# Kernel tuning notes

Hardware: AMD Instinct MI355X
Metric: run time of the kernel (lower is better)

Reference implementation:

```python
import jax, jax.numpy as jnp
import numpy as np

B, H, W, C = 16, 256, 256, 32
FILTER = 64


def conv_relu(x, k, b):
    y = jax.lax.conv_general_dilated(x, k, (1, 1), 'VALID',
                                     dimension_numbers=('NHWC', 'HWIO', 'NHWC'))
    return jax.nn.relu(y + b)


def maxpool2(x):
    return jax.lax.reduce_window(x, -jnp.inf, jax.lax.max,
                                 (1, 2, 2, 1), (1, 2, 2, 1), 'VALID')


def affine_grid_generator(theta):
    # tf.meshgrid default 'xy': shapes [W, H]
    xs = jnp.linspace(-1.0, 1.0, H)
    ys = jnp.linspace(-1.0, 1.0, W)
    xT, yT = jnp.meshgrid(xs, ys)
    grid = jnp.stack([xT.ravel(), yT.ravel(), jnp.ones(W * H, jnp.float32)])  # [3, W*H]
    batch_grid = jnp.einsum('bij,jk->bik', theta, grid)  # [B,2,W*H]
    return batch_grid.reshape(B, 2, H, W)


def get_pixel_value(fm, xi, yi):
    b = jnp.arange(B)[:, None, None]
    return fm[b, yi, xi]  # [B,H,W,C]


def bilinear_sampler(fm, x, y):
    max_x = H - 1
    max_y = W - 1
    x = 0.5 * ((x + 1.0) * jnp.float32(max_x - 1))
    y = 0.5 * ((y + 1.0) * jnp.float32(max_y - 1))
    x0 = jnp.floor(x).astype(jnp.int32)
    x1 = x0 + 1
    y0 = jnp.floor(y).astype(jnp.int32)
    y1 = y0 + 1
    x0 = jnp.clip(x0, 0, max_x)
    x1 = jnp.clip(x1, 0, max_x)
    y0 = jnp.clip(y0, 0, max_y)
    y1 = jnp.clip(y1, 0, max_y)
    Ia = get_pixel_value(fm, x0, y0)
    Ib = get_pixel_value(fm, x0, y1)
    Ic = get_pixel_value(fm, x1, y0)
    Id = get_pixel_value(fm, x1, y1)
    x0f, x1f = x0.astype(jnp.float32), x1.astype(jnp.float32)
    y0f, y1f = y0.astype(jnp.float32), y1.astype(jnp.float32)
    wa = ((x1f - x) * (y1f - y))[..., None]
    wb = ((x1f - x) * (y - y0f))[..., None]
    wc = ((x - x0f) * (y1f - y))[..., None]
    wd = ((x - x0f) * (y - y0f))[..., None]
    return wa * Ia + wb * Ib + wc * Ic + wd * Id


def setup_inputs() -> dict:
    key = jax.random.key(0)
    ks = jax.random.split(key, 12)

    def he(k, shape, fan_in):
        return jax.random.normal(k, shape, jnp.float32) * np.sqrt(2.0 / fan_in)

    f4, f2 = FILTER // 4, FILTER // 2
    x = jax.random.normal(ks[0], (B, H, W, C), jnp.float32)
    W1 = he(ks[1], (3, 3, C, f4), 9 * C); b1 = jnp.zeros((f4,), jnp.float32)
    W2 = he(ks[2], (3, 3, f4, f2), 9 * f4); b2 = jnp.zeros((f2,), jnp.float32)
    W3 = he(ks[3], (3, 3, f2, f2), 9 * f2); b3 = jnp.zeros((f2,), jnp.float32)
    D1 = he(ks[4], (f2, FILTER), f2); db1 = jnp.zeros((FILTER,), jnp.float32)
    D2 = he(ks[5], (FILTER, f2), FILTER); db2 = jnp.zeros((f2,), jnp.float32)
    # original inits kernel to zeros, bias to identity transform; use small
    # random kernel so the sampled grid is a non-trivial near-identity warp.
    D3 = jax.random.normal(ks[6], (f2, 6), jnp.float32) * 0.01
    db3 = jnp.array([1.0, 0.0, 0.0, 0.0, 1.0, 0.0], jnp.float32)
    return {"x": x, "W1": W1, "b1": b1, "W2": W2, "b2": b2, "W3": W3, "b3": b3,
            "D1": D1, "db1": db1, "D2": D2, "db2": db2, "D3": D3, "db3": db3}


def reference(x, W1, b1, W2, b2, W3, b3, D1, db1, D2, db2, D3, db3):
    # localization net
    h = maxpool2(conv_relu(x, W1, b1))
    h = maxpool2(conv_relu(h, W2, b2))
    h = maxpool2(conv_relu(h, W3, b3))
    h = jnp.mean(h, axis=(1, 2))  # GlobalAveragePooling2D -> [B, filter//2]
    h = jax.nn.relu(h @ D1 + db1)
    h = jax.nn.relu(h @ D2 + db2)
    theta = (h @ D3 + db3).reshape(B, 2, 3)
    grid = affine_grid_generator(theta)
    xS = grid[:, 0]
    yS = grid[:, 1]
    return bilinear_sampler(x, xS, yS)
```

## Files before the change

kernel.cpp:

```cpp
#include <hip/hip_runtime.h>
#include <hip/hip_bf16.h>


#define P1_ELEMS 4129024
#define P2_ELEMS 1968128
#define P3_ELEMS 460800

#define C1_ROWS 10
#define C1_COLS 34

__global__ __launch_bounds__(256) void conv1_pool_kernel(
    const float* __restrict__ x, const float* __restrict__ W1,
    const float* __restrict__ b1, float* __restrict__ p1)
{
    __shared__ float xt[C1_ROWS * C1_COLS * 32];
    __shared__ float wlds[3*3*32*16];

    const int tid = threadIdx.x;
    for (int i = tid; i < 3*3*32*16; i += 256) wlds[i] = W1[i];

    const int b   = blockIdx.z;
    const int ph0 = blockIdx.y * 4;
    const int pw0 = blockIdx.x * 16;
    const float* xb = x + (size_t)b * (256*256*32);

    for (int i = tid; i < C1_ROWS * C1_COLS * 8; i += 256) {
        const int dr  = i / (C1_COLS * 8);
        const int rem = i - dr * (C1_COLS * 8);
        const int j   = rem >> 3;
        const int ch  = rem & 7;
        int r_in = 2*ph0 + dr; if (r_in > 255) r_in = 255;
        int c_in = 2*pw0 + j;  if (c_in > 255) c_in = 255;
        const float4 v = *(const float4*)(xb + ((size_t)r_in*256 + c_in)*32 + ch*4);
        const int slot = (ch + (j >> 1)) & 7;
        *(float4*)(&xt[(dr * C1_COLS + j) * 32 + slot * 4]) = v;
    }
    __syncthreads();

    const int fq  = tid & 3;
    const int pix = tid >> 2;
    const int row = pix >> 4;
    const int col = pix & 15;
    const int lr  = 2 * row;
    const int lc  = 2 * col;

    float4 acc[4];
    {
        const float4 bv = *(const float4*)(b1 + 4*fq);
        acc[0] = bv; acc[1] = bv; acc[2] = bv; acc[3] = bv;
    }

    for (int kh = 0; kh < 3; ++kh)
    for (int kw = 0; kw < 3; ++kw) {
        #pragma unroll
        for (int c4 = 0; c4 < 8; ++c4) {
            float4 xv[4];
            #pragma unroll
            for (int p = 0; p < 4; ++p) {
                const int rr   = lr + (p >> 1) + kh;
                const int jj   = lc + (p & 1) + kw;
                const int slot = (c4 + (jj >> 1)) & 7;
                xv[p] = *(const float4*)(&xt[(rr * C1_COLS + jj) * 32 + slot * 4]);
            }
            const float* wp_ = &wlds[((kh*3 + kw)*32 + c4*4) * 16 + 4*fq];
            #pragma unroll
            for (int cc = 0; cc < 4; ++cc) {
                const float4 w4 = *(const float4*)(wp_ + cc*16);
                #pragma unroll
                for (int p = 0; p < 4; ++p) {
                    const float xc = (cc == 0) ? xv[p].x : (cc == 1) ? xv[p].y
                                   : (cc == 2) ? xv[p].z : xv[p].w;
                    acc[p].x += xc * w4.x;
                    acc[p].y += xc * w4.y;
                    acc[p].z += xc * w4.z;
                    acc[p].w += xc * w4.w;
                }
            }
        }
    }

    const int ph = ph0 + row, pw = pw0 + col;
    if (ph < 127 && pw < 127) {
        float4 o;
        o.x = fmaxf(fmaxf(fmaxf(acc[0].x, acc[1].x), fmaxf(acc[2].x, acc[3].x)), 0.0f);
        o.y = fmaxf(fmaxf(fmaxf(acc[0].y, acc[1].y), fmaxf(acc[2].y, acc[3].y)), 0.0f);
        o.z = fmaxf(fmaxf(fmaxf(acc[0].z, acc[1].z), fmaxf(acc[2].z, acc[3].z)), 0.0f);
        o.w = fmaxf(fmaxf(fmaxf(acc[0].w, acc[1].w), fmaxf(acc[2].w, acc[3].w)), 0.0f);
        *(float4*)(p1 + (((size_t)b*127 + ph)*127 + pw) * 16 + 4*fq) = o;
    }
}

__global__ __launch_bounds__(256) void conv2_pool_kernel(
    const float* __restrict__ p1, const float* __restrict__ W2,
    const float* __restrict__ b2, float* __restrict__ p2)
{
    __shared__ float wlds[3*3*16*32];
    for (int i = threadIdx.x; i < 3*3*16*32; i += 256) wlds[i] = W2[i];
    __syncthreads();

    const int b   = blockIdx.z;
    const int tid = threadIdx.x;
    const int fg  = tid >> 7;
    const int rem = tid & 127;
    const int ph  = blockIdx.y * 8  + (rem >> 4);
    const int pw  = blockIdx.x * 16 + (rem & 15);
    const bool valid = (ph < 62) && (pw < 62);
    const int hp = valid ? ph : 61;
    const int wp = valid ? pw : 61;

    const float* xb = p1 + (size_t)b * (127*127*16);
    const int h0 = 2*hp, w0 = 2*wp;

    float acc[4][16];
    #pragma unroll
    for (int f = 0; f < 16; ++f) {
        float bv = b2[fg*16 + f];
        acc[0][f]=bv; acc[1][f]=bv; acc[2][f]=bv; acc[3][f]=bv;
    }

    for (int kh = 0; kh < 3; ++kh)
    for (int kw = 0; kw < 3; ++kw) {
        #pragma unroll
        for (int c4 = 0; c4 < 4; ++c4) {
            float xr[4][4];
            #pragma unroll
            for (int p = 0; p < 4; ++p) {
                const int hh = h0 + (p >> 1) + kh;
                const int ww = w0 + (p & 1) + kw;
                const float4 xv = *(const float4*)(xb + ((size_t)hh*127 + ww)*16 + c4*4);
                xr[p][0]=xv.x; xr[p][1]=xv.y; xr[p][2]=xv.z; xr[p][3]=xv.w;
            }
            #pragma unroll
            for (int cc = 0; cc < 4; ++cc) {
                const float* wb_ = &wlds[((kh*3 + kw)*16 + c4*4 + cc) * 32 + fg*16];
                float wv[16];
                #pragma unroll
                for (int q = 0; q < 4; ++q) {
                    const float4 w4 = *(const float4*)(wb_ + 4*q);
                    wv[4*q+0]=w4.x; wv[4*q+1]=w4.y; wv[4*q+2]=w4.z; wv[4*q+3]=w4.w;
                }
                #pragma unroll
                for (int p = 0; p < 4; ++p) {
                    const float xc = xr[p][cc];
                    #pragma unroll
                    for (int f = 0; f < 16; ++f) acc[p][f] += xc * wv[f];
                }
            }
        }
    }

    if (valid) {
        float out[16];
        #pragma unroll
        for (int f = 0; f < 16; ++f) {
            float m = fmaxf(fmaxf(acc[0][f], acc[1][f]), fmaxf(acc[2][f], acc[3][f]));
            out[f] = fmaxf(m, 0.0f);
        }
        float* dst = p2 + (((size_t)b*62 + ph)*62 + pw) * 32 + fg*16;
        #pragma unroll
        for (int q = 0; q < 4; ++q)
            *(float4*)(dst + 4*q) = make_float4(out[4*q], out[4*q+1], out[4*q+2], out[4*q+3]);
    }
}

__global__ __launch_bounds__(256) void conv3_pool_kernel(
    const float* __restrict__ p2, const float* __restrict__ W3,
    const float* __restrict__ b3, float* __restrict__ p3)
{
    __shared__ float wlds[3*3*32*32];
    for (int i = threadIdx.x; i < 3*3*32*32; i += 256) wlds[i] = W3[i];
    __syncthreads();

    const int b   = blockIdx.z;
    const int tid = threadIdx.x;
    const int fg  = tid >> 7;
    const int rem = tid & 127;
    const int ph  = blockIdx.y * 8  + (rem >> 4);
    const int pw  = blockIdx.x * 16 + (rem & 15);
    const bool valid = (ph < 30) && (pw < 30);
    const int hp = valid ? ph : 29;
    const int wp = valid ? pw : 29;

    const float* xb = p2 + (size_t)b * (62*62*32);
    const int h0 = 2*hp, w0 = 2*wp;

    float acc[4][16];
    #pragma unroll
    for (int f = 0; f < 16; ++f) {
        float bv = b3[fg*16 + f];
        acc[0][f]=bv; acc[1][f]=bv; acc[2][f]=bv; acc[3][f]=bv;
    }

    for (int kh = 0; kh < 3; ++kh)
    for (int kw = 0; kw < 3; ++kw) {
        #pragma unroll
        for (int c4 = 0; c4 < 8; ++c4) {
            float xr[4][4];
            #pragma unroll
            for (int p = 0; p < 4; ++p) {
                const int hh = h0 + (p >> 1) + kh;
                const int ww = w0 + (p & 1) + kw;
                const float4 xv = *(const float4*)(xb + ((size_t)hh*62 + ww)*32 + c4*4);
                xr[p][0]=xv.x; xr[p][1]=xv.y; xr[p][2]=xv.z; xr[p][3]=xv.w;
            }
            #pragma unroll
            for (int cc = 0; cc < 4; ++cc) {
                const float* wb_ = &wlds[((kh*3 + kw)*32 + c4*4 + cc) * 32 + fg*16];
                float wv[16];
                #pragma unroll
                for (int q = 0; q < 4; ++q) {
                    const float4 w4 = *(const float4*)(wb_ + 4*q);
                    wv[4*q+0]=w4.x; wv[4*q+1]=w4.y; wv[4*q+2]=w4.z; wv[4*q+3]=w4.w;
                }
                #pragma unroll
                for (int p = 0; p < 4; ++p) {
                    const float xc = xr[p][cc];
                    #pragma unroll
                    for (int f = 0; f < 16; ++f) acc[p][f] += xc * wv[f];
                }
            }
        }
    }

    if (valid) {
        float out[16];
        #pragma unroll
        for (int f = 0; f < 16; ++f) {
            float m = fmaxf(fmaxf(acc[0][f], acc[1][f]), fmaxf(acc[2][f], acc[3][f]));
            out[f] = fmaxf(m, 0.0f);
        }
        float* dst = p3 + (((size_t)b*30 + ph)*30 + pw) * 32 + fg*16;
        #pragma unroll
        for (int q = 0; q < 4; ++q)
            *(float4*)(dst + 4*q) = make_float4(out[4*q], out[4*q+1], out[4*q+2], out[4*q+3]);
    }
}

__global__ __launch_bounds__(256) void head_kernel(
    const float* __restrict__ p3,
    const float* __restrict__ D1, const float* __restrict__ db1,
    const float* __restrict__ D2, const float* __restrict__ db2,
    const float* __restrict__ D3, const float* __restrict__ db3,
    float* __restrict__ theta)
{
    __shared__ float red[8][32];
    __shared__ float hmean[32];
    __shared__ float h1[64];
    __shared__ float h2[32];

    const int b   = blockIdx.x;
    const int tid = threadIdx.x;
    const int c = tid & 31, r = tid >> 5;

    const float* p = p3 + (size_t)b * (900*32);
    float s = 0.0f;
    for (int i = r; i < 900; i += 8) s += p[i*32 + c];
    red[r][c] = s;
    __syncthreads();

    if (tid < 32) {
        float m = 0.0f;
        #pragma unroll
        for (int j = 0; j < 8; ++j) m += red[j][tid];
        hmean[tid] = m * (1.0f / 900.0f);
    }
    __syncthreads();

    if (tid < 64) {
        float a = db1[tid];
        #pragma unroll
        for (int k = 0; k < 32; ++k) a += hmean[k] * D1[k*64 + tid];
        h1[tid] = fmaxf(a, 0.0f);
    }
    __syncthreads();

    if (tid < 32) {
        float a = db2[tid];
        #pragma unroll
        for (int k = 0; k < 64; ++k) a += h1[k] * D2[k*32 + tid];
        h2[tid] = fmaxf(a, 0.0f);
    }
    __syncthreads();

    if (tid < 6) {
        float a = db3[tid];
        #pragma unroll
        for (int k = 0; k < 32; ++k) a += h2[k] * D3[k*6 + tid];
        theta[b*6 + tid] = a;
    }
}

__global__ __launch_bounds__(256) void sampler_kernel(
    const float* __restrict__ x, const float* __restrict__ theta,
    float* __restrict__ out)
{
    const int t  = blockIdx.x * 256 + threadIdx.x;
    const int c4 = t & 7;
    const int w  = (t >> 3) & 255;
    const int h  = (t >> 11) & 255;
    const int b  = t >> 19;

    const float* th = theta + b*6;
    const float gx = -1.0f + (float)w * (2.0f / 255.0f);
    const float gy = -1.0f + (float)h * (2.0f / 255.0f);
    const float xS = th[0]*gx + th[1]*gy + th[2];
    const float yS = th[3]*gx + th[4]*gy + th[5];
    const float xp = 0.5f * (xS + 1.0f) * 254.0f;
    const float yp = 0.5f * (yS + 1.0f) * 254.0f;

    int x0 = (int)floorf(xp), y0 = (int)floorf(yp);
    int x1 = x0 + 1,          y1 = y0 + 1;
    x0 = x0 < 0 ? 0 : (x0 > 255 ? 255 : x0);
    x1 = x1 < 0 ? 0 : (x1 > 255 ? 255 : x1);
    y0 = y0 < 0 ? 0 : (y0 > 255 ? 255 : y0);
    y1 = y1 < 0 ? 0 : (y1 > 255 ? 255 : y1);

    const float x0f = (float)x0, x1f = (float)x1;
    const float y0f = (float)y0, y1f = (float)y1;
    const float wa = (x1f - xp) * (y1f - yp);
    const float wb = (x1f - xp) * (yp - y0f);
    const float wc = (xp - x0f) * (y1f - yp);
    const float wd = (xp - x0f) * (yp - y0f);

    const float* xb = x + (size_t)b * (256*256*32) + c4*4;
    const float4 Ia = *(const float4*)(xb + ((size_t)y0*256 + x0)*32);
    const float4 Ib = *(const float4*)(xb + ((size_t)y1*256 + x0)*32);
    const float4 Ic = *(const float4*)(xb + ((size_t)y0*256 + x1)*32);
    const float4 Id = *(const float4*)(xb + ((size_t)y1*256 + x1)*32);

    float4 o;
    o.x = wa*Ia.x + wb*Ib.x + wc*Ic.x + wd*Id.x;
    o.y = wa*Ia.y + wb*Ib.y + wc*Ic.y + wd*Id.y;
    o.z = wa*Ia.z + wb*Ib.z + wc*Ic.z + wd*Id.z;
    o.w = wa*Ia.w + wb*Ib.w + wc*Ic.w + wd*Id.w;
    ((float4*)out)[t] = o;
}

extern "C" void kernel_launch(void* const* d_in, const int* in_sizes, int n_in,
                              void* d_out, int out_size, void* d_ws, size_t ws_size,
                              hipStream_t stream) {
    const float* x   = (const float*)d_in[0];
    const float* W1  = (const float*)d_in[1];
    const float* b1  = (const float*)d_in[2];
    const float* W2  = (const float*)d_in[3];
    const float* b2  = (const float*)d_in[4];
    const float* W3  = (const float*)d_in[5];
    const float* b3  = (const float*)d_in[6];
    const float* D1  = (const float*)d_in[7];
    const float* db1 = (const float*)d_in[8];
    const float* D2  = (const float*)d_in[9];
    const float* db2 = (const float*)d_in[10];
    const float* D3  = (const float*)d_in[11];
    const float* db3 = (const float*)d_in[12];
    float* out = (float*)d_out;

    float* p1    = (float*)d_ws;
    float* p2    = p1 + P1_ELEMS;
    float* p3    = p2 + P2_ELEMS;
    float* theta = p3 + P3_ELEMS;

    conv1_pool_kernel<<<dim3(8, 32, 16), 256, 0, stream>>>(x,  W1, b1, p1);
    conv2_pool_kernel<<<dim3(4, 8, 16),  256, 0, stream>>>(p1, W2, b2, p2);
    conv3_pool_kernel<<<dim3(2, 4, 16),  256, 0, stream>>>(p2, W3, b3, p3);
    head_kernel      <<<dim3(16),        256, 0, stream>>>(p3, D1, db1, D2, db2, D3, db3, theta);
    sampler_kernel   <<<dim3(32768),     256, 0, stream>>>(x, theta, out);
}
```

Baseline: 522.9 us.

## Restructure conv kernels: wave-uniform filter groups, LDS input tiles, scalar weight loads

```diff
diff --git a/kernel.cpp b/kernel.cpp
--- a/kernel.cpp
+++ b/kernel.cpp
@@ -6,160 +6,180 @@
 #define P2_ELEMS 1968128
 #define P3_ELEMS 460800
 
-#define C1_ROWS 10
-#define C1_COLS 34
+#define C1_PXSTR 36
+#define C1_ROWSTR (34*36)
 
 __global__ __launch_bounds__(256) void conv1_pool_kernel(
     const float* __restrict__ x, const float* __restrict__ W1,
     const float* __restrict__ b1, float* __restrict__ p1)
 {
-    __shared__ float xt[C1_ROWS * C1_COLS * 32];
-    __shared__ float wlds[3*3*32*16];
+    __shared__ float xt[10 * C1_ROWSTR];
 
     const int tid = threadIdx.x;
-    for (int i = tid; i < 3*3*32*16; i += 256) wlds[i] = W1[i];
-
     const int b   = blockIdx.z;
     const int ph0 = blockIdx.y * 4;
     const int pw0 = blockIdx.x * 16;
     const float* xb = x + (size_t)b * (256*256*32);
 
-    for (int i = tid; i < C1_ROWS * C1_COLS * 8; i += 256) {
-        const int dr  = i / (C1_COLS * 8);
-        const int rem = i - dr * (C1_COLS * 8);
+    for (int i = tid; i < 10*34*8; i += 256) {
+        const int dr  = i / 272;
+        const int rem = i - dr * 272;
         const int j   = rem >> 3;
         const int ch  = rem & 7;
         int r_in = 2*ph0 + dr; if (r_in > 255) r_in = 255;
         int c_in = 2*pw0 + j;  if (c_in > 255) c_in = 255;
         const float4 v = *(const float4*)(xb + ((size_t)r_in*256 + c_in)*32 + ch*4);
-        const int slot = (ch + (j >> 1)) & 7;
-        *(float4*)(&xt[(dr * C1_COLS + j) * 32 + slot * 4]) = v;
-    }
-    __syncthreads();
-
-    const int fq  = tid & 3;
-    const int pix = tid >> 2;
-    const int row = pix >> 4;
-    const int col = pix & 15;
-    const int lr  = 2 * row;
-    const int lc  = 2 * col;
-
-    float4 acc[4];
+        *(float4*)(&xt[dr*C1_ROWSTR + j*C1_PXSTR + ch*4]) = v;
+    }
+    __syncthreads();
+
+    const int fq   = __builtin_amdgcn_readfirstlane(tid >> 6);
+    const int lane = tid & 63;
+    const int row  = lane >> 4;
+    const int col  = lane & 15;
+
+    float4 a0, a1, a2, a3;
     {
         const float4 bv = *(const float4*)(b1 + 4*fq);
-        acc[0] = bv; acc[1] = bv; acc[2] = bv; acc[3] = bv;
-    }
-
-    for (int kh = 0; kh < 3; ++kh)
-    for (int kw = 0; kw < 3; ++kw) {
+        a0 = bv; a1 = bv; a2 = bv; a3 = bv;
+    }
+
+    const float* xbase = &xt[(2*row)*C1_ROWSTR + (2*col)*C1_PXSTR];
+    const float* wbase = W1 + 4*fq;
+
+#define C1_FMA(A, XV) \
+    A.x += XV.x*w0.x; A.y += XV.x*w0.y; A.z += XV.x*w0.z; A.w += XV.x*w0.w; \
+    A.x += XV.y*w1.x; A.y += XV.y*w1.y; A.z += XV.y*w1.z; A.w += XV.y*w1.w; \
+    A.x += XV.z*w2.x; A.y += XV.z*w2.y; A.z += XV.z*w2.z; A.w += XV.z*w2.w; \
+    A.x += XV.w*w3.x; A.y += XV.w*w3.y; A.z += XV.w*w3.z; A.w += XV.w*w3.w;
+
+    #pragma unroll 1
+    for (int kh = 0; kh < 3; ++kh) {
+      #pragma unroll 1
+      for (int kw = 0; kw < 3; ++kw) {
+        const float* xp_ = xbase + kh*C1_ROWSTR + kw*C1_PXSTR;
+        const float* wp_ = wbase + (kh*3 + kw)*32*16;
         #pragma unroll
         for (int c4 = 0; c4 < 8; ++c4) {
-            float4 xv[4];
-            #pragma unroll
-            for (int p = 0; p < 4; ++p) {
-                const int rr   = lr + (p >> 1) + kh;
-                const int jj   = lc + (p & 1) + kw;
-                const int slot = (c4 + (jj >> 1)) & 7;
-                xv[p] = *(const float4*)(&xt[(rr * C1_COLS + jj) * 32 + slot * 4]);
-            }
-            const float* wp_ = &wlds[((kh*3 + kw)*32 + c4*4) * 16 + 4*fq];
-            #pragma unroll
-            for (int cc = 0; cc < 4; ++cc) {
-                const float4 w4 = *(const float4*)(wp_ + cc*16);
-                #pragma unroll
-                for (int p = 0; p < 4; ++p) {
-                    const float xc = (cc == 0) ? xv[p].x : (cc == 1) ? xv[p].y
-                                   : (cc == 2) ? xv[p].z : xv[p].w;
-                    acc[p].x += xc * w4.x;
-                    acc[p].y += xc * w4.y;
-                    acc[p].z += xc * w4.z;
-                    acc[p].w += xc * w4.w;
-                }
-            }
+            const float4 x0 = *(const float4*)(xp_ + 4*c4);
+            const float4 x1 = *(const float4*)(xp_ + C1_PXSTR + 4*c4);
+            const float4 x2 = *(const float4*)(xp_ + C1_ROWSTR + 4*c4);
+            const float4 x3 = *(const float4*)(xp_ + C1_ROWSTR + C1_PXSTR + 4*c4);
+            const float4 w0 = *(const float4*)(wp_ + (4*c4+0)*16);
+            const float4 w1 = *(const float4*)(wp_ + (4*c4+1)*16);
+            const float4 w2 = *(const float4*)(wp_ + (4*c4+2)*16);
+            const float4 w3 = *(const float4*)(wp_ + (4*c4+3)*16);
+            C1_FMA(a0, x0)
+            C1_FMA(a1, x1)
+            C1_FMA(a2, x2)
+            C1_FMA(a3, x3)
         }
+      }
     }
 
     const int ph = ph0 + row, pw = pw0 + col;
     if (ph < 127 && pw < 127) {
         float4 o;
-        o.x = fmaxf(fmaxf(fmaxf(acc[0].x, acc[1].x), fmaxf(acc[2].x, acc[3].x)), 0.0f);
-        o.y = fmaxf(fmaxf(fmaxf(acc[0].y, acc[1].y), fmaxf(acc[2].y, acc[3].y)), 0.0f);
-        o.z = fmaxf(fmaxf(fmaxf(acc[0].z, acc[1].z), fmaxf(acc[2].z, acc[3].z)), 0.0f);
-        o.w = fmaxf(fmaxf(fmaxf(acc[0].w, acc[1].w), fmaxf(acc[2].w, acc[3].w)), 0.0f);
+        o.x = fmaxf(fmaxf(fmaxf(a0.x, a1.x), fmaxf(a2.x, a3.x)), 0.0f);
+        o.y = fmaxf(fmaxf(fmaxf(a0.y, a1.y), fmaxf(a2.y, a3.y)), 0.0f);
+        o.z = fmaxf(fmaxf(fmaxf(a0.z, a1.z), fmaxf(a2.z, a3.z)), 0.0f);
+        o.w = fmaxf(fmaxf(fmaxf(a0.w, a1.w), fmaxf(a2.w, a3.w)), 0.0f);
         *(float4*)(p1 + (((size_t)b*127 + ph)*127 + pw) * 16 + 4*fq) = o;
     }
 }
+
+#define C2_PXSTR 20
+#define C2_ROWSTR (34*20)
 
 __global__ __launch_bounds__(256) void conv2_pool_kernel(
     const float* __restrict__ p1, const float* __restrict__ W2,
     const float* __restrict__ b2, float* __restrict__ p2)
 {
-    __shared__ float wlds[3*3*16*32];
-    for (int i = threadIdx.x; i < 3*3*16*32; i += 256) wlds[i] = W2[i];
-    __syncthreads();
-
+    __shared__ float xt[10 * C2_ROWSTR];
+
+    const int tid = threadIdx.x;
     const int b   = blockIdx.z;
-    const int tid = threadIdx.x;
-    const int fg  = tid >> 7;
-    const int rem = tid & 127;
-    const int ph  = blockIdx.y * 8  + (rem >> 4);
-    const int pw  = blockIdx.x * 16 + (rem & 15);
-    const bool valid = (ph < 62) && (pw < 62);
-    const int hp = valid ? ph : 61;
-    const int wp = valid ? pw : 61;
-
+    const int ph0 = blockIdx.y * 4;
+    const int pw0 = blockIdx.x * 16;
     const float* xb = p1 + (size_t)b * (127*127*16);
-    const int h0 = 2*hp, w0 = 2*wp;
-
-    float acc[4][16];
-    #pragma unroll
-    for (int f = 0; f < 16; ++f) {
-        float bv = b2[fg*16 + f];
-        acc[0][f]=bv; acc[1][f]=bv; acc[2][f]=bv; acc[3][f]=bv;
-    }
-
-    for (int kh = 0; kh < 3; ++kh)
-    for (int kw = 0; kw < 3; ++kw) {
+
+    for (int i = tid; i < 10*34*4; i += 256) {
+        const int dr  = i / 136;
+        const int rem = i - dr * 136;
+        const int j   = rem >> 2;
+        const int ch  = rem & 3;
+        int r_in = 2*ph0 + dr; if (r_in > 126) r_in = 126;
+        int c_in = 2*pw0 + j;  if (c_in > 126) c_in = 126;
+        const float4 v = *(const float4*)(xb + ((size_t)r_in*127 + c_in)*16 + ch*4);
+        *(float4*)(&xt[dr*C2_ROWSTR + j*C2_PXSTR + ch*4]) = v;
+    }
+    __syncthreads();
+
+    const int wv   = __builtin_amdgcn_readfirstlane(tid >> 6);
+    const int lane = tid & 63;
+    const int row  = lane >> 4;
+    const int col  = lane & 15;
+    const int f0   = 8 * wv;
+
+    float4 aA0, aA1, aA2, aA3;
+    float4 aB0, aB1, aB2, aB3;
+    {
+        const float4 bvA = *(const float4*)(b2 + f0);
+        const float4 bvB = *(const float4*)(b2 + f0 + 4);
+        aA0 = bvA; aA1 = bvA; aA2 = bvA; aA3 = bvA;
+        aB0 = bvB; aB1 = bvB; aB2 = bvB; aB3 = bvB;
+    }
+
+    const float* xbase = &xt[(2*row)*C2_ROWSTR + (2*col)*C2_PXSTR];
+    const float* wbase = W2 + f0;
+
+#define C2_FMA(AA, AB, XC, WA, WB) \
+    AA.x += XC*WA.x; AA.y += XC*WA.y; AA.z += XC*WA.z; AA.w += XC*WA.w; \
+    AB.x += XC*WB.x; AB.y += XC*WB.y; AB.z += XC*WB.z; AB.w += XC*WB.w;
+
+    #pragma unroll 1
+    for (int kh = 0; kh < 3; ++kh) {
+      #pragma unroll 1
+      for (int kw = 0; kw < 3; ++kw) {
+        const float* xp_ = xbase + kh*C2_ROWSTR + kw*C2_PXSTR;
+        const float* wp_ = wbase + (kh*3 + kw)*16*32;
         #pragma unroll
         for (int c4 = 0; c4 < 4; ++c4) {
-            float xr[4][4];
+            const float4 x0 = *(const float4*)(xp_ + 4*c4);
+            const float4 x1 = *(const float4*)(xp_ + C2_PXSTR + 4*c4);
+            const float4 x2 = *(const float4*)(xp_ + C2_ROWSTR + 4*c4);
+            const float4 x3 = *(const float4*)(xp_ + C2_ROWSTR + C2_PXSTR + 4*c4);
             #pragma unroll
-            for (int p = 0; p < 4; ++p) {
-                const int hh = h0 + (p >> 1) + kh;
-                const int ww = w0 + (p & 1) + kw;
-                const float4 xv = *(const float4*)(xb + ((size_t)hh*127 + ww)*16 + c4*4);
-                xr[p][0]=xv.x; xr[p][1]=xv.y; xr[p][2]=xv.z; xr[p][3]=xv.w;
-            }
-            #pragma unroll
-            for (int cc = 0; cc < 4; ++cc) {
-                const float* wb_ = &wlds[((kh*3 + kw)*16 + c4*4 + cc) * 32 + fg*16];
-                float wv[16];
-                #pragma unroll
-                for (int q = 0; q < 4; ++q) {
-                    const float4 w4 = *(const float4*)(wb_ + 4*q);
-                    wv[4*q+0]=w4.x; wv[4*q+1]=w4.y; wv[4*q+2]=w4.z; wv[4*q+3]=w4.w;
-                }
-                #pragma unroll
-                for (int p = 0; p < 4; ++p) {
-                    const float xc = xr[p][cc];
-                    #pragma unroll
-                    for (int f = 0; f < 16; ++f) acc[p][f] += xc * wv[f];
-                }
+            for (int c = 0; c < 4; ++c) {
+                const float4 wA = *(const float4*)(wp_ + (4*c4+c)*32);
+                const float4 wB = *(const float4*)(wp_ + (4*c4+c)*32 + 4);
+                const float xc0 = (c==0)?x0.x:(c==1)?x0.y:(c==2)?x0.z:x0.w;
+                const float xc1 = (c==0)?x1.x:(c==1)?x1.y:(c==2)?x1.z:x1.w;
+                const float xc2 = (c==0)?x2.x:(c==1)?x2.y:(c==2)?x2.z:x2.w;
+                const float xc3 = (c==0)?x3.x:(c==1)?x3.y:(c==2)?x3.z:x3.w;
+                C2_FMA(aA0, aB0, xc0, wA, wB)
+                C2_FMA(aA1, aB1, xc1, wA, wB)
+                C2_FMA(aA2, aB2, xc2, wA, wB)
+                C2_FMA(aA3, aB3, xc3, wA, wB)
             }
         }
-    }
-
-    if (valid) {
-        float out[16];
-        #pragma unroll
-        for (int f = 0; f < 16; ++f) {
-            float m = fmaxf(fmaxf(acc[0][f], acc[1][f]), fmaxf(acc[2][f], acc[3][f]));
-            out[f] = fmaxf(m, 0.0f);
-        }
-        float* dst = p2 + (((size_t)b*62 + ph)*62 + pw) * 32 + fg*16;
-        #pragma unroll
-        for (int q = 0; q < 4; ++q)
-            *(float4*)(dst + 4*q) = make_float4(out[4*q], out[4*q+1], out[4*q+2], out[4*q+3]);
+      }
+    }
+
+    const int ph = ph0 + row, pw = pw0 + col;
+    if (ph < 62 && pw < 62) {
+        float4 oA, oB;
+        oA.x = fmaxf(fmaxf(fmaxf(aA0.x, aA1.x), fmaxf(aA2.x, aA3.x)), 0.0f);
+        oA.y = fmaxf(fmaxf(fmaxf(aA0.y, aA1.y), fmaxf(aA2.y, aA3.y)), 0.0f);
+        oA.z = fmaxf(fmaxf(fmaxf(aA0.z, aA1.z), fmaxf(aA2.z, aA3.z)), 0.0f);
+        oA.w = fmaxf(fmaxf(fmaxf(aA0.w, aA1.w), fmaxf(aA2.w, aA3.w)), 0.0f);
+        oB.x = fmaxf(fmaxf(fmaxf(aB0.x, aB1.x), fmaxf(aB2.x, aB3.x)), 0.0f);
+        oB.y = fmaxf(fmaxf(fmaxf(aB0.y, aB1.y), fmaxf(aB2.y, aB3.y)), 0.0f);
+        oB.z = fmaxf(fmaxf(fmaxf(aB0.z, aB1.z), fmaxf(aB2.z, aB3.z)), 0.0f);
+        oB.w = fmaxf(fmaxf(fmaxf(aB0.w, aB1.w), fmaxf(aB2.w, aB3.w)), 0.0f);
+        float* dst = p2 + (((size_t)b*62 + ph)*62 + pw) * 32 + f0;
+        *(float4*)(dst)     = oA;
+        *(float4*)(dst + 4) = oB;
     }
 }
 
@@ -167,72 +187,87 @@
     const float* __restrict__ p2, const float* __restrict__ W3,
     const float* __restrict__ b3, float* __restrict__ p3)
 {
-    __shared__ float wlds[3*3*32*32];
-    for (int i = threadIdx.x; i < 3*3*32*32; i += 256) wlds[i] = W3[i];
-    __syncthreads();
-
+    __shared__ float xt[10 * C1_ROWSTR];
+
+    const int tid = threadIdx.x;
     const int b   = blockIdx.z;
-    const int tid = threadIdx.x;
-    const int fg  = tid >> 7;
-    const int rem = tid & 127;
-    const int ph  = blockIdx.y * 8  + (rem >> 4);
-    const int pw  = blockIdx.x * 16 + (rem & 15);
-    const bool valid = (ph < 30) && (pw < 30);
-    const int hp = valid ? ph : 29;
-    const int wp = valid ? pw : 29;
-
+    const int ph0 = blockIdx.y * 4;
+    const int pw0 = blockIdx.x * 16;
     const float* xb = p2 + (size_t)b * (62*62*32);
-    const int h0 = 2*hp, w0 = 2*wp;
-
-    float acc[4][16];
-    #pragma unroll
-    for (int f = 0; f < 16; ++f) {
-        float bv = b3[fg*16 + f];
-        acc[0][f]=bv; acc[1][f]=bv; acc[2][f]=bv; acc[3][f]=bv;
-    }
-
-    for (int kh = 0; kh < 3; ++kh)
-    for (int kw = 0; kw < 3; ++kw) {
+
+    for (int i = tid; i < 10*34*8; i += 256) {
+        const int dr  = i / 272;
+        const int rem = i - dr * 272;
+        const int j   = rem >> 3;
+        const int ch  = rem & 7;
+        int r_in = 2*ph0 + dr; if (r_in > 61) r_in = 61;
+        int c_in = 2*pw0 + j;  if (c_in > 61) c_in = 61;
+        const float4 v = *(const float4*)(xb + ((size_t)r_in*62 + c_in)*32 + ch*4);
+        *(float4*)(&xt[dr*C1_ROWSTR + j*C1_PXSTR + ch*4]) = v;
+    }
+    __syncthreads();
+
+    const int wv   = __builtin_amdgcn_readfirstlane(tid >> 6);
+    const int lane = tid & 63;
+    const int row  = lane >> 4;
+    const int col  = lane & 15;
+    const int f0   = 8 * wv;
+
+    float4 aA0, aA1, aA2, aA3;
+    float4 aB0, aB1, aB2, aB3;
+    {
+        const float4 bvA = *(const float4*)(b3 + f0);
+        const float4 bvB = *(const float4*)(b3 + f0 + 4);
+        aA0 = bvA; aA1 = bvA; aA2 = bvA; aA3 = bvA;
+        aB0 = bvB; aB1 = bvB; aB2 = bvB; aB3 = bvB;
+    }
+
+    const float* xbase = &xt[(2*row)*C1_ROWSTR + (2*col)*C1_PXSTR];
+    const float* wbase = W3 + f0;
+
+    #pragma unroll 1
+    for (int kh = 0; kh < 3; ++kh) {
+      #pragma unroll 1
+      for (int kw = 0; kw < 3; ++kw) {
+        const float* xp_ = xbase + kh*C1_ROWSTR + kw*C1_PXSTR;
+        const float* wp_ = wbase + (kh*3 + kw)*32*32;
         #pragma unroll
         for (int c4 = 0; c4 < 8; ++c4) {
-            float xr[4][4];
+            const float4 x0 = *(const float4*)(xp_ + 4*c4);
+            const float4 x1 = *(const float4*)(xp_ + C1_PXSTR + 4*c4);
+            const float4 x2 = *(const float4*)(xp_ + C1_ROWSTR + 4*c4);
+            const float4 x3 = *(const float4*)(xp_ + C1_ROWSTR + C1_PXSTR + 4*c4);
             #pragma unroll
-            for (int p = 0; p < 4; ++p) {
-                const int hh = h0 + (p >> 1) + kh;
-                const int ww = w0 + (p & 1) + kw;
-                const float4 xv = *(const float4*)(xb + ((size_t)hh*62 + ww)*32 + c4*4);
-                xr[p][0]=xv.x; xr[p][1]=xv.y; xr[p][2]=xv.z; xr[p][3]=xv.w;
-            }
-            #pragma unroll
-            for (int cc = 0; cc < 4; ++cc) {
-                const float* wb_ = &wlds[((kh*3 + kw)*32 + c4*4 + cc) * 32 + fg*16];
-                float wv[16];
-                #pragma unroll
-                for (int q = 0; q < 4; ++q) {
-                    const float4 w4 = *(const float4*)(wb_ + 4*q);
-                    wv[4*q+0]=w4.x; wv[4*q+1]=w4.y; wv[4*q+2]=w4.z; wv[4*q+3]=w4.w;
-                }
-                #pragma unroll
-                for (int p = 0; p < 4; ++p) {
-                    const float xc = xr[p][cc];
-                    #pragma unroll
-                    for (int f = 0; f < 16; ++f) acc[p][f] += xc * wv[f];
-                }
+            for (int c = 0; c < 4; ++c) {
+                const float4 wA = *(const float4*)(wp_ + (4*c4+c)*32);
+                const float4 wB = *(const float4*)(wp_ + (4*c4+c)*32 + 4);
+                const float xc0 = (c==0)?x0.x:(c==1)?x0.y:(c==2)?x0.z:x0.w;
+                const float xc1 = (c==0)?x1.x:(c==1)?x1.y:(c==2)?x1.z:x1.w;
+                const float xc2 = (c==0)?x2.x:(c==1)?x2.y:(c==2)?x2.z:x2.w;
+                const float xc3 = (c==0)?x3.x:(c==1)?x3.y:(c==2)?x3.z:x3.w;
+                C2_FMA(aA0, aB0, xc0, wA, wB)
+                C2_FMA(aA1, aB1, xc1, wA, wB)
+                C2_FMA(aA2, aB2, xc2, wA, wB)
+                C2_FMA(aA3, aB3, xc3, wA, wB)
             }
         }
-    }
-
-    if (valid) {
-        float out[16];
-        #pragma unroll
-        for (int f = 0; f < 16; ++f) {
-            float m = fmaxf(fmaxf(acc[0][f], acc[1][f]), fmaxf(acc[2][f], acc[3][f]));
-            out[f] = fmaxf(m, 0.0f);
-        }
-        float* dst = p3 + (((size_t)b*30 + ph)*30 + pw) * 32 + fg*16;
-        #pragma unroll
-        for (int q = 0; q < 4; ++q)
-            *(float4*)(dst + 4*q) = make_float4(out[4*q], out[4*q+1], out[4*q+2], out[4*q+3]);
+      }
+    }
+
+    const int ph = ph0 + row, pw = pw0 + col;
+    if (ph < 30 && pw < 30) {
+        float4 oA, oB;
+        oA.x = fmaxf(fmaxf(fmaxf(aA0.x, aA1.x), fmaxf(aA2.x, aA3.x)), 0.0f);
+        oA.y = fmaxf(fmaxf(fmaxf(aA0.y, aA1.y), fmaxf(aA2.y, aA3.y)), 0.0f);
+        oA.z = fmaxf(fmaxf(fmaxf(aA0.z, aA1.z), fmaxf(aA2.z, aA3.z)), 0.0f);
+        oA.w = fmaxf(fmaxf(fmaxf(aA0.w, aA1.w), fmaxf(aA2.w, aA3.w)), 0.0f);
+        oB.x = fmaxf(fmaxf(fmaxf(aB0.x, aB1.x), fmaxf(aB2.x, aB3.x)), 0.0f);
+        oB.y = fmaxf(fmaxf(fmaxf(aB0.y, aB1.y), fmaxf(aB2.y, aB3.y)), 0.0f);
+        oB.z = fmaxf(fmaxf(fmaxf(aB0.z, aB1.z), fmaxf(aB2.z, aB3.z)), 0.0f);
+        oB.w = fmaxf(fmaxf(fmaxf(aB0.w, aB1.w), fmaxf(aB2.w, aB3.w)), 0.0f);
+        float* dst = p3 + (((size_t)b*30 + ph)*30 + pw) * 32 + f0;
+        *(float4*)(dst)     = oA;
+        *(float4*)(dst + 4) = oB;
     }
 }
 
@@ -360,8 +395,8 @@
     float* theta = p3 + P3_ELEMS;
 
     conv1_pool_kernel<<<dim3(8, 32, 16), 256, 0, stream>>>(x,  W1, b1, p1);
-    conv2_pool_kernel<<<dim3(4, 8, 16),  256, 0, stream>>>(p1, W2, b2, p2);
-    conv3_pool_kernel<<<dim3(2, 4, 16),  256, 0, stream>>>(p2, W3, b3, p3);
+    conv2_pool_kernel<<<dim3(4, 16, 16), 256, 0, stream>>>(p1, W2, b2, p2);
+    conv3_pool_kernel<<<dim3(2, 8, 16),  256, 0, stream>>>(p2, W3, b3, p3);
     head_kernel      <<<dim3(16),        256, 0, stream>>>(p3, D1, db1, D2, db2, D3, db3, theta);
     sampler_kernel   <<<dim3(32768),     256, 0, stream>>>(x, theta, out);
 }
```

Result: faster. 487.2 us (-6.8%).
